# Performance work log

Measured on AMD Instinct MI355X. Metric: run time of the kernel, lower is better.

## Reference

```python
import jax, jax.numpy as jnp
import numpy as np

DIM = 512
HEADS = 8
DIM_HEAD = 64
ROT_DIM = DIM_HEAD // 2  # RotaryEmbedding(dim_head // 2)
B = 4
N = 8192


def rotate_every_two(x):
    # '... (d j) -> ... d j', j=2 ; (x1, x2) -> (-x2, x1) interleaved back
    x1 = x[..., 0::2]
    x2 = x[..., 1::2]
    return jnp.stack((-x2, x1), axis=-1).reshape(x.shape)


def apply_rotary_emb(freqs, t):
    # freqs: [1,1,n,rot_dim]; rotary on first rot_dim channels, passthrough rest
    rot_dim = freqs.shape[-1]
    t_rot, t_pass = t[..., :rot_dim], t[..., rot_dim:]
    t_rot = t_rot * jnp.cos(freqs) + rotate_every_two(t_rot) * jnp.sin(freqs)
    return jnp.concatenate((t_rot, t_pass), axis=-1)


def rotary_freqs(n):
    # lucidrains RotaryEmbedding(ROT_DIM): inv_freq over ROT_DIM//2, repeated r=2
    inv_freq = 1.0 / (10000.0 ** (jnp.arange(0, ROT_DIM, 2, dtype=jnp.float32) / ROT_DIM))
    f = jnp.arange(n, dtype=jnp.float32)[:, None] * inv_freq[None, :]  # [n, ROT_DIM//2]
    return jnp.repeat(f, 2, axis=-1)  # [n, ROT_DIM]


def setup_inputs() -> dict:
    key = jax.random.key(0)
    ks = jax.random.split(key, 8)
    inner = HEADS * DIM_HEAD
    s = lambda fan_in: 1.0 / np.sqrt(fan_in)
    return {
        "x": jax.random.normal(ks[0], (B, N, DIM), dtype=jnp.float32),
        "w_qkv": jax.random.uniform(ks[1], (DIM, inner * 3), jnp.float32, -s(DIM), s(DIM)),
        "w_q_logits": jax.random.uniform(ks[2], (DIM_HEAD, 1), jnp.float32, -s(DIM_HEAD), s(DIM_HEAD)),
        "w_k_logits": jax.random.uniform(ks[3], (DIM_HEAD // 2, 1), jnp.float32, -s(DIM_HEAD // 2), s(DIM_HEAD // 2)),
        "w_r": jax.random.uniform(ks[4], (DIM_HEAD // 2, DIM_HEAD), jnp.float32, -s(DIM_HEAD // 2), s(DIM_HEAD // 2)),
        "b_r": jax.random.uniform(ks[5], (DIM_HEAD,), jnp.float32, -s(DIM_HEAD // 2), s(DIM_HEAD // 2)),
        "w_out": jax.random.uniform(ks[6], (inner, DIM), jnp.float32, -s(inner), s(inner)),
        "b_out": jax.random.uniform(ks[7], (DIM,), jnp.float32, -s(inner), s(inner)),
    }


def reference(x, w_qkv, w_q_logits, w_k_logits, w_r, b_r, w_out, b_out):
    b, n, _ = x.shape
    h, d = HEADS, DIM_HEAD
    scale = d ** -0.5

    qkv = x @ w_qkv  # [b,n,3*h*d]
    q, k, v = jnp.split(qkv, 3, axis=-1)
    to_bhnd = lambda t: t.reshape(b, n, h, d).transpose(0, 2, 1, 3)
    q, k, v = to_bhnd(q), to_bhnd(k), to_bhnd(v)

    freqs = rotary_freqs(n)[None, None]  # [1,1,n,ROT_DIM]
    q_aggr = apply_rotary_emb(freqs, q)
    k_aggr = apply_rotary_emb(freqs, k)
    v_aggr = v

    q_attn = jax.nn.softmax((q @ w_q_logits)[..., 0] * scale, axis=-1)  # [b,h,n]
    global_q = jnp.einsum('bhn,bhnd->bhd', q_attn, q_aggr)[:, :, None]  # [b,h,1,d]

    kk = (k * global_q).reshape(b, h, n, d // 2, 2).sum(-1)  # sum adjacent pairs -> [b,h,n,d/2]
    k_attn = jax.nn.softmax((kk @ w_k_logits)[..., 0] * scale, axis=-1)
    global_k = jnp.einsum('bhn,bhnd->bhd', k_attn, k_aggr)[:, :, None]  # [b,h,1,d]

    u = (v_aggr * global_k).reshape(b, h, n, d // 2, 2).sum(-1)  # [b,h,n,d/2]
    r = u @ w_r + b_r  # [b,h,n,d]
    r = r + q
    r = r.transpose(0, 2, 1, 3).reshape(b, n, h * d)
    return r @ w_out + b_out
```

## Files before the change

### kernel.cpp

```cpp
#include <hip/hip_runtime.h>
#include <hip/hip_bf16.h>

typedef __attribute__((ext_vector_type(8))) short s16x8;
typedef __attribute__((ext_vector_type(4))) short s16x4;
typedef __attribute__((ext_vector_type(4))) float f32x4;

#define SEQ 8192

__device__ __forceinline__ float bf2f(short s){
  union { unsigned u; float f; } c; c.u = ((unsigned)(unsigned short)s) << 16; return c.f;
}
__device__ __forceinline__ short f2bf(float f){
  __hip_bfloat16 h = __float2bfloat16(f);
  short s; __builtin_memcpy(&s, &h, 2); return s;
}

__global__ __launch_bounds__(256) void build_tab64(float* __restrict__ ct, float* __restrict__ st){
  int idx = blockIdx.x*256 + threadIdx.x;
  int n = idx >> 6, d = idx & 63;
  float c, s;
  if (d < 32){
    float ex = -(float)(d & ~1) / 32.0f;
    float invf = __expf(ex * 9.210340371976184f);
    float f = (float)n * invf;
    c = cosf(f);
    s = sinf(f);
    s = (d & 1) ? s : -s;
  } else { c = 1.f; s = 0.f; }
  ct[idx] = c; st[idx] = s;
}

__global__ __launch_bounds__(256) void cvt_x(const float* __restrict__ in, __hip_bfloat16* __restrict__ out){
  int i = blockIdx.x*256 + threadIdx.x;
  float4 v = reinterpret_cast<const float4*>(in)[i];
  s16x4 o = { f2bf(v.x), f2bf(v.y), f2bf(v.z), f2bf(v.w) };
  reinterpret_cast<s16x4*>(out)[i] = o;
}

__global__ __launch_bounds__(256) void transpose_cvt(const float* __restrict__ in, __hip_bfloat16* __restrict__ out,
                                                     int R, int C){
  __shared__ float tile[32][33];
  int c0 = blockIdx.x*32, r0 = blockIdx.y*32;
  int tx = threadIdx.x & 31, ty = threadIdx.x >> 5;
  #pragma unroll
  for (int i = ty; i < 32; i += 8) tile[i][tx] = in[(size_t)(r0+i)*C + c0 + tx];
  __syncthreads();
  #pragma unroll
  for (int i = ty; i < 32; i += 8) out[(size_t)(c0+i)*R + r0 + tx] = __float2bfloat16(tile[tx][i]);
}

#define FENCE_BAR() do { asm volatile("" ::: "memory"); __builtin_amdgcn_s_barrier(); \
                         __builtin_amdgcn_sched_barrier(0); } while(0)

template<int MODE>
__global__ __launch_bounds__(512, 2) void gemm256(
    const __hip_bfloat16* __restrict__ A, const __hip_bfloat16* __restrict__ BT,
    int M, int Nn, int K,
    __hip_bfloat16* __restrict__ oQ, __hip_bfloat16* __restrict__ oK, __hip_bfloat16* __restrict__ oV,
    float* __restrict__ oF, const float* __restrict__ bias)
{
  __shared__ __align__(16) char lds[131072];
  const int t = threadIdx.x;
  const int lane = t & 63, wid = t >> 6;
  const int lr = lane & 15, lg = lane >> 4;
  const int wm128 = (wid >> 2) * 128;
  const int wn64  = (wid & 3) * 64;

  int nwg = gridDim.x, per = nwg >> 3, wg = blockIdx.x;
  int swz = (wg & 7) * per + (wg >> 3);
  int mblk = M >> 8;
  int bm = (swz % mblk) << 8;
  int bn = (swz / mblk) << 8;

  const int NKT = K >> 6;

  const __hip_bfloat16* sp[8];
  int dOff[8];
  #pragma unroll
  for (int i = 0; i < 8; ++i){
    int g = t + i*512;
    int row = g >> 3;
    int dch = (g & 7) ^ (row & 7);
    sp[i] = (i < 4 ? A + (size_t)(bm + row)*K
                   : BT + (size_t)(bn + row - 256)*K) + dch*8;
    dOff[i] = g * 16;
  }

  #define STG(i, kn, buf) __builtin_amdgcn_global_load_lds( \
      (const __attribute__((address_space(1))) void*)(sp[i] + (kn)*64), \
      (__attribute__((address_space(3))) void*)(lds + (buf)*65536 + dOff[i]), 16, 0, 0)

  #pragma unroll
  for (int i = 0; i < 8; ++i) STG(i, 0, 0);
  asm volatile("s_waitcnt vmcnt(0)" ::: "memory");
  __builtin_amdgcn_s_barrier();
  __builtin_amdgcn_sched_barrier(0);

  f32x4 acc[8][4] = {};
  s16x8 af[4], bf[4];

  #define LREAD(base, r, cb) (*reinterpret_cast<const s16x8*>((base) + ((r) << 7) + (((cb)) ^ (((r) & 7) << 4))))
  #define RD_A(h, ks) _Pragma("unroll") \
    for (int f = 0; f < 4; ++f){ int r = wm128 + (h)*64 + f*16 + lr; af[f] = LREAD(lb, r, (ks)*64 + lg*16); }
  #define RD_B(ks) _Pragma("unroll") \
    for (int f = 0; f < 4; ++f){ int r = 256 + wn64 + f*16 + lr; bf[f] = LREAD(lb, r, (ks)*64 + lg*16); }
  #define MFMA16(h) do { __builtin_amdgcn_s_setprio(1); \
    _Pragma("unroll") for (int m2 = 0; m2 < 4; ++m2) \
    _Pragma("unroll") for (int ni = 0; ni < 4; ++ni){ \
      if (MODE == 0) acc[(h)*4+m2][ni] = __builtin_amdgcn_mfma_f32_16x16x32_bf16(bf[ni], af[m2], acc[(h)*4+m2][ni], 0, 0, 0); \
      else           acc[(h)*4+m2][ni] = __builtin_amdgcn_mfma_f32_16x16x32_bf16(af[m2], bf[ni], acc[(h)*4+m2][ni], 0, 0, 0); } \
    __builtin_amdgcn_s_setprio(0); } while(0)

  for (int kt = 0; kt < NKT; ++kt){
    const char* lb = lds + (kt & 1)*65536;
    const int sb = (kt & 1) ^ 1;
    const int kn = kt + 1;
    const bool stg = kn < NKT;
    RD_A(0, 0); RD_B(0);
    if (stg){ STG(0, kn, sb); STG(1, kn, sb); }
    FENCE_BAR();
    MFMA16(0);
    FENCE_BAR();
    RD_A(1, 0);
    if (stg){ STG(2, kn, sb); STG(3, kn, sb); }
    FENCE_BAR();
    MFMA16(1);
    FENCE_BAR();
    RD_A(0, 1); RD_B(1);
    if (stg){ STG(4, kn, sb); STG(5, kn, sb); }
    FENCE_BAR();
    MFMA16(0);
    FENCE_BAR();
    RD_A(1, 1);
    if (stg){ STG(6, kn, sb); STG(7, kn, sb); }
    FENCE_BAR();
    MFMA16(1);
    asm volatile("s_waitcnt vmcnt(0)" ::: "memory");
    __builtin_amdgcn_s_barrier();
    __builtin_amdgcn_sched_barrier(0);
  }

  if (MODE == 0){
    char* reg = lds + wid*16384;
    #pragma unroll
    for (int mi = 0; mi < 8; ++mi){
      #pragma unroll
      for (int ni = 0; ni < 4; ++ni){
        int tok = mi*16 + lr;
        int cb = (ni*16 + lg*4) * 2;
        ushort4 w4;
        w4.x = (unsigned short)f2bf(acc[mi][ni][0]);
        w4.y = (unsigned short)f2bf(acc[mi][ni][1]);
        w4.z = (unsigned short)f2bf(acc[mi][ni][2]);
        w4.w = (unsigned short)f2bf(acc[mi][ni][3]);
        *reinterpret_cast<unsigned long long*>(reg + tok*128 + (cb ^ ((tok & 7) << 3))) =
            *reinterpret_cast<unsigned long long*>(&w4);
      }
    }
    int gcol = bn + wn64;
    int ts = gcol >> 9, rem = gcol & 511, h = rem >> 6;
    __hip_bfloat16* dstT = (ts == 0) ? oQ : ((ts == 1) ? oK : oV);
    int tokbase = bm + wm128;
    int bb = tokbase >> 13;
    dstT += ((size_t)(bb*8 + h)) << 19;
    #pragma unroll
    for (int p2 = 0; p2 < 16; ++p2){
      int tok = p2*8 + (lane >> 3);
      int b0 = (lane & 7) * 16;
      int sw = (tok & 7) << 3;
      unsigned long long u0 = *reinterpret_cast<const unsigned long long*>(reg + tok*128 + (b0 ^ sw));
      unsigned long long u1 = *reinterpret_cast<const unsigned long long*>(reg + tok*128 + ((b0 + 8) ^ sw));
      int n = (tokbase + tok) & 8191;
      unsigned long long o2[2] = { u0, u1 };
      *reinterpret_cast<s16x8*>(dstT + ((size_t)n << 6) + (lane & 7)*8) =
          *reinterpret_cast<const s16x8*>(o2);
    }
  } else {
    #pragma unroll
    for (int mi = 0; mi < 8; ++mi){
      #pragma unroll
      for (int ni = 0; ni < 4; ++ni){
        int gc = bn + wn64 + ni*16 + lr;
        float bv = bias[gc];
        #pragma unroll
        for (int j = 0; j < 4; ++j){
          int gr = bm + wm128 + mi*16 + lg*4 + j;
          oF[(size_t)gr*Nn + gc] = acc[mi][ni][j] + bv;
        }
      }
    }
  }
  #undef STG
  #undef LREAD
  #undef RD_A
  #undef RD_B
  #undef MFMA16
}

__global__ __launch_bounds__(256) void fused_stats(
    const __hip_bfloat16* __restrict__ T, const float* __restrict__ svec, int svstride, float scale,
    const float* __restrict__ ct, const float* __restrict__ st, float* __restrict__ outp)
{
  int chunk = blockIdx.x, bh = blockIdx.y;
  int t = threadIdx.x, lane = t & 63, w = t >> 6;
  __shared__ float sv[64];
  __shared__ float ev[256];
  __shared__ float redv[4][64];
  __shared__ float rede[4];
  if (t < 64) sv[t] = svec[svstride*bh + t] * scale;
  __syncthreads();

  int n = chunk*256 + t;
  const __hip_bfloat16* row = T + ((size_t)bh*SEQ + n)*64;
  float s = 0.f;
  #pragma unroll
  for (int dv = 0; dv < 8; ++dv){
    s16x8 v8 = *reinterpret_cast<const s16x8*>(row + dv*8);
    #pragma unroll
    for (int e = 0; e < 8; ++e) s += bf2f(v8[e]) * sv[dv*8 + e];
  }
  ev[t] = __expf(s);
  __syncthreads();

  const short* Tsh = reinterpret_cast<const short*>(T + ((size_t)bh*SEQ)*64);
  float acc = 0.f, se = 0.f;
  int nb = chunk*256 + w*64;
  #pragma unroll 4
  for (int i = 0; i < 64; ++i){
    int n2 = nb + i;
    float e = ev[w*64 + i];
    float xv = bf2f(Tsh[(size_t)n2*64 + lane]);
    float xo = __shfl_xor(xv, 1, 64);
    acc += e * (xv*ct[n2*64 + lane] + xo*st[n2*64 + lane]);
    se += e;
  }
  redv[w][lane] = acc;
  if (lane == 0) rede[w] = se;
  __syncthreads();
  if (t < 64){
    float* ob = outp + (size_t)(bh*32 + chunk)*66;
    ob[2 + t] = redv[0][t] + redv[1][t] + redv[2][t] + redv[3][t];
    if (t == 0) ob[1] = rede[0] + rede[1] + rede[2] + rede[3];
  }
}

__global__ void final_combine(const float* __restrict__ parts, float* __restrict__ gvec,
                              const float* __restrict__ wkl, float* __restrict__ gqwk)
{
  int bh = blockIdx.x, d = threadIdx.x;
  const float* pp = parts + (size_t)bh*32*66;
  float tot = 0.f, g = 0.f;
  #pragma unroll 4
  for (int i = 0; i < 32; ++i){ tot += pp[i*66 + 1]; g += pp[i*66 + 2 + d]; }
  g /= tot;
  gvec[bh*64 + d] = g;
  if (gqwk) gqwk[bh*64 + d] = g * wkl[d >> 1] * 0.125f;
}

__global__ __launch_bounds__(256) void epilogue_r(
    const __hip_bfloat16* __restrict__ vT, const __hip_bfloat16* __restrict__ qT,
    const float* __restrict__ gk, const float* __restrict__ wr, const float* __restrict__ br,
    __hip_bfloat16* __restrict__ rb)
{
  int idx = blockIdx.x*256 + threadIdx.x;
  int bh = idx >> 13, nl = idx & 8191;
  int b = bh >> 3, h = bh & 7;
  const __hip_bfloat16* vrow = vT + (size_t)idx*64;
  const __hip_bfloat16* qrow = qT + (size_t)idx*64;
  const float* gkb = gk + bh*64;
  float u[32];
  #pragma unroll
  for (int dv = 0; dv < 8; ++dv){
    s16x8 v8 = *reinterpret_cast<const s16x8*>(vrow + dv*8);
    #pragma unroll
    for (int e = 0; e < 8; e += 2){
      int d = dv*8 + e;
      u[d >> 1] = bf2f(v8[e])*gkb[d] + bf2f(v8[e+1])*gkb[d+1];
    }
  }
  __hip_bfloat16* rrow = rb + ((size_t)(b*SEQ + nl))*512 + h*64;
  #pragma unroll 2
  for (int dv = 0; dv < 8; ++dv){
    s16x8 q8 = *reinterpret_cast<const s16x8*>(qrow + dv*8);
    s16x8 o8;
    #pragma unroll
    for (int e = 0; e < 8; ++e){
      int d = dv*8 + e;
      float a2 = br[d] + bf2f(q8[e]);
      #pragma unroll
      for (int j = 0; j < 32; ++j) a2 += u[j] * wr[j*64 + d];
      o8[e] = f2bf(a2);
    }
    *reinterpret_cast<s16x8*>(rrow + dv*8) = o8;
  }
}

extern "C" void kernel_launch(void* const* d_in, const int* in_sizes, int n_in,
                              void* d_out, int out_size, void* d_ws, size_t ws_size,
                              hipStream_t stream)
{
  (void)in_sizes; (void)n_in; (void)out_size; (void)ws_size;
  const float* x    = (const float*)d_in[0];
  const float* wqkv = (const float*)d_in[1];
  const float* wql  = (const float*)d_in[2];
  const float* wkl  = (const float*)d_in[3];
  const float* wr   = (const float*)d_in[4];
  const float* br   = (const float*)d_in[5];
  const float* wout = (const float*)d_in[6];
  const float* bout = (const float*)d_in[7];
  float* out = (float*)d_out;

  char* p = (char*)d_ws;
  auto alloc = [&](size_t bytes){ char* r = p; p += (bytes + 255) & ~(size_t)255; return r; };
  __hip_bfloat16* xb    = (__hip_bfloat16*)alloc(33554432);
  __hip_bfloat16* wqkvT = (__hip_bfloat16*)alloc(1572864);
  __hip_bfloat16* woutT = (__hip_bfloat16*)alloc(524288);
  __hip_bfloat16* qT = (__hip_bfloat16*)alloc(33554432);
  __hip_bfloat16* kT = (__hip_bfloat16*)alloc(33554432);
  __hip_bfloat16* vT = (__hip_bfloat16*)alloc(33554432);
  __hip_bfloat16* rb = (__hip_bfloat16*)alloc(33554432);
  float* ct     = (float*)alloc(2097152);
  float* st     = (float*)alloc(2097152);
  float* gq     = (float*)alloc(8192);
  float* gqwk   = (float*)alloc(8192);
  float* gk     = (float*)alloc(8192);

  float* partsQ = (float*)xb;
  float* partsK = partsQ + 32*32*66;

  build_tab64<<<2048, 256, 0, stream>>>(ct, st);
  cvt_x<<<16384, 256, 0, stream>>>(x, xb);
  transpose_cvt<<<dim3(48,16), 256, 0, stream>>>(wqkv, wqkvT, 512, 1536);
  transpose_cvt<<<dim3(16,16), 256, 0, stream>>>(wout, woutT, 512, 512);

  gemm256<0><<<768, 512, 0, stream>>>(xb, wqkvT, 32768, 1536, 512,
                                      qT, kT, vT, nullptr, nullptr);

  fused_stats<<<dim3(32,32), 256, 0, stream>>>(qT, wql, 0, 0.125f, ct, st, partsQ);
  final_combine<<<32, 64, 0, stream>>>(partsQ, gq, wkl, gqwk);
  fused_stats<<<dim3(32,32), 256, 0, stream>>>(kT, gqwk, 64, 1.0f, ct, st, partsK);
  final_combine<<<32, 64, 0, stream>>>(partsK, gk, nullptr, nullptr);

  epilogue_r<<<1024, 256, 0, stream>>>(vT, qT, gk, wr, br, rb);

  gemm256<1><<<256, 512, 0, stream>>>(rb, woutT, 32768, 512, 512,
                                      nullptr, nullptr, nullptr, out, bout);
}
```

Measured before the change: 216.8 us.

## Restructure GEMM mainloop to 4-stage K=32 LDS pipeline with single barrier

Replaces the double-buffered K=64 GEMM mainloop, which used several barriers per tile, with a 4-slot ring of K=32 tiles. Loads run three tiles ahead, and progress is gated by graded vmcnt waits plus one barrier per iteration. It also changes the LDS swizzle and switches block rasterization from M-major to N-major. The goal is to hide global-load latency and cut barrier overhead, at the cost of shorter MFMA bursts per barrier and more iterations.

```diff
diff --git a/kernel.cpp b/kernel.cpp
--- a/kernel.cpp
+++ b/kernel.cpp
@@ -49,9 +49,6 @@
   for (int i = ty; i < 32; i += 8) out[(size_t)(c0+i)*R + r0 + tx] = __float2bfloat16(tile[tx][i]);
 }
 
-#define FENCE_BAR() do { asm volatile("" ::: "memory"); __builtin_amdgcn_s_barrier(); \
-                         __builtin_amdgcn_sched_barrier(0); } while(0)
-
 template<int MODE>
 __global__ __launch_bounds__(512, 2) void gemm256(
     const __hip_bfloat16* __restrict__ A, const __hip_bfloat16* __restrict__ BT,
@@ -68,77 +65,62 @@
 
   int nwg = gridDim.x, per = nwg >> 3, wg = blockIdx.x;
   int swz = (wg & 7) * per + (wg >> 3);
-  int mblk = M >> 8;
-  int bm = (swz % mblk) << 8;
-  int bn = (swz / mblk) << 8;
-
-  const int NKT = K >> 6;
-
-  const __hip_bfloat16* sp[8];
-  int dOff[8];
-  #pragma unroll
-  for (int i = 0; i < 8; ++i){
-    int g = t + i*512;
-    int row = g >> 3;
-    int dch = (g & 7) ^ (row & 7);
-    sp[i] = (i < 4 ? A + (size_t)(bm + row)*K
-                   : BT + (size_t)(bn + row - 256)*K) + dch*8;
-    dOff[i] = g * 16;
-  }
-
-  #define STG(i, kn, buf) __builtin_amdgcn_global_load_lds( \
-      (const __attribute__((address_space(1))) void*)(sp[i] + (kn)*64), \
-      (__attribute__((address_space(3))) void*)(lds + (buf)*65536 + dOff[i]), 16, 0, 0)
-
-  #pragma unroll
-  for (int i = 0; i < 8; ++i) STG(i, 0, 0);
-  asm volatile("s_waitcnt vmcnt(0)" ::: "memory");
-  __builtin_amdgcn_s_barrier();
-  __builtin_amdgcn_sched_barrier(0);
+  int nblk = Nn >> 8;
+  int bm = (swz / nblk) << 8;
+  int bn = (swz % nblk) << 8;
+
+  const int NKT = K >> 5;
+
+  const __hip_bfloat16* spp[4];
+  int dofs[4];
+  #pragma unroll
+  for (int i = 0; i < 4; ++i){
+    int g = t + (i & 1)*512;
+    int row = g >> 2, ch = g & 3;
+    int sch = ch ^ ((row & 3) ^ ((row >> 2) & 3));
+    spp[i] = (i < 2 ? A + (size_t)(bm + row)*K : BT + (size_t)(bn + row)*K) + sch*8;
+    dofs[i] = ((i < 2) ? 0 : 16384) + g*16;
+  }
+  #define STG(i, kt) __builtin_amdgcn_global_load_lds( \
+      (const __attribute__((address_space(1))) void*)(spp[i] + (size_t)(kt)*32), \
+      (__attribute__((address_space(3))) void*)(lds + (((kt) & 3) << 15) + dofs[i]), 16, 0, 0)
+
+  #pragma unroll
+  for (int tl = 0; tl < 3; ++tl){ STG(0, tl); STG(1, tl); STG(2, tl); STG(3, tl); }
 
   f32x4 acc[8][4] = {};
-  s16x8 af[4], bf[4];
-
-  #define LREAD(base, r, cb) (*reinterpret_cast<const s16x8*>((base) + ((r) << 7) + (((cb)) ^ (((r) & 7) << 4))))
-  #define RD_A(h, ks) _Pragma("unroll") \
-    for (int f = 0; f < 4; ++f){ int r = wm128 + (h)*64 + f*16 + lr; af[f] = LREAD(lb, r, (ks)*64 + lg*16); }
-  #define RD_B(ks) _Pragma("unroll") \
-    for (int f = 0; f < 4; ++f){ int r = 256 + wn64 + f*16 + lr; bf[f] = LREAD(lb, r, (ks)*64 + lg*16); }
-  #define MFMA16(h) do { __builtin_amdgcn_s_setprio(1); \
-    _Pragma("unroll") for (int m2 = 0; m2 < 4; ++m2) \
-    _Pragma("unroll") for (int ni = 0; ni < 4; ++ni){ \
-      if (MODE == 0) acc[(h)*4+m2][ni] = __builtin_amdgcn_mfma_f32_16x16x32_bf16(bf[ni], af[m2], acc[(h)*4+m2][ni], 0, 0, 0); \
-      else           acc[(h)*4+m2][ni] = __builtin_amdgcn_mfma_f32_16x16x32_bf16(af[m2], bf[ni], acc[(h)*4+m2][ni], 0, 0, 0); } \
-    __builtin_amdgcn_s_setprio(0); } while(0)
+  #define SWB(r) ((((r) & 3) ^ (((r) >> 2) & 3)) << 4)
 
   for (int kt = 0; kt < NKT; ++kt){
-    const char* lb = lds + (kt & 1)*65536;
-    const int sb = (kt & 1) ^ 1;
-    const int kn = kt + 1;
-    const bool stg = kn < NKT;
-    RD_A(0, 0); RD_B(0);
-    if (stg){ STG(0, kn, sb); STG(1, kn, sb); }
-    FENCE_BAR();
-    MFMA16(0);
-    FENCE_BAR();
-    RD_A(1, 0);
-    if (stg){ STG(2, kn, sb); STG(3, kn, sb); }
-    FENCE_BAR();
-    MFMA16(1);
-    FENCE_BAR();
-    RD_A(0, 1); RD_B(1);
-    if (stg){ STG(4, kn, sb); STG(5, kn, sb); }
-    FENCE_BAR();
-    MFMA16(0);
-    FENCE_BAR();
-    RD_A(1, 1);
-    if (stg){ STG(6, kn, sb); STG(7, kn, sb); }
-    FENCE_BAR();
-    MFMA16(1);
-    asm volatile("s_waitcnt vmcnt(0)" ::: "memory");
+    if (kt + 2 < NKT)       asm volatile("s_waitcnt vmcnt(8)" ::: "memory");
+    else if (kt + 2 == NKT) asm volatile("s_waitcnt vmcnt(4)" ::: "memory");
+    else                    asm volatile("s_waitcnt vmcnt(0)" ::: "memory");
     __builtin_amdgcn_s_barrier();
     __builtin_amdgcn_sched_barrier(0);
-  }
+    const char* lb = lds + ((kt & 3) << 15);
+    s16x8 af[8], bfr[4];
+    #pragma unroll
+    for (int mi = 0; mi < 8; ++mi){
+      int r = wm128 + mi*16 + lr;
+      af[mi] = *reinterpret_cast<const s16x8*>(lb + r*64 + ((lg << 4) ^ SWB(r)));
+    }
+    #pragma unroll
+    for (int ni = 0; ni < 4; ++ni){
+      int r = wn64 + ni*16 + lr;
+      bfr[ni] = *reinterpret_cast<const s16x8*>(lb + 16384 + r*64 + ((lg << 4) ^ SWB(r)));
+    }
+    if (kt + 3 < NKT){ STG(0, kt+3); STG(1, kt+3); STG(2, kt+3); STG(3, kt+3); }
+    __builtin_amdgcn_s_setprio(1);
+    #pragma unroll
+    for (int mi = 0; mi < 8; ++mi)
+      #pragma unroll
+      for (int ni = 0; ni < 4; ++ni){
+        if (MODE == 0) acc[mi][ni] = __builtin_amdgcn_mfma_f32_16x16x32_bf16(bfr[ni], af[mi], acc[mi][ni], 0, 0, 0);
+        else           acc[mi][ni] = __builtin_amdgcn_mfma_f32_16x16x32_bf16(af[mi], bfr[ni], acc[mi][ni], 0, 0, 0);
+      }
+    __builtin_amdgcn_s_setprio(0);
+  }
+  __builtin_amdgcn_s_barrier();
 
   if (MODE == 0){
     char* reg = lds + wid*16384;
@@ -191,10 +173,7 @@
     }
   }
   #undef STG
-  #undef LREAD
-  #undef RD_A
-  #undef RD_B
-  #undef MFMA16
+  #undef SWB
 }
 
 __global__ __launch_bounds__(256) void fused_stats(
```

After: 211.0 us. 2.7% less time.
